# Kernel optimization log

Measured on AMD Instinct MI355X. Metric: run time of the kernel, lower is better.

## Reference

```python
import jax, jax.numpy as jnp
import numpy as np

B, T, M, D, K, L = 128, 50, 4, 64, 64, 16  # batch, seq len, num_beh, embed dim, num_classes, capsule_length
NUM_ITEMS = 100000
R_ITERS = 3


def _dyn_gru(x, C, Wx, bx, Wh, bh):
    """Dynamic capsule GRU. x: [B,M,T,D], C: [B,M,T,K,L] (routing state modulates update gate).
    Returns final hidden beh_e [B,M,K,L] and per-step candidate states beh_N [B,M,T,K,L]."""
    # precompute input projections for all steps: [B,M,T,3,K,L]
    gi = (jnp.einsum('bmtd,mdg->bmtg', x, Wx) + bx[:, None, :]).reshape(x.shape[0], M, T, 3, K, L)

    def step(h, inp):
        gi_t, C_t = inp  # gi_t: [B,M,3,K,L], C_t: [B,M,K,L]
        gh = (jnp.einsum('bmkl,mklg->bmkg', h, Wh) + bh).reshape(h.shape[0], M, K, 3, L)
        r = jax.nn.sigmoid(gi_t[:, :, 0] + gh[:, :, :, 0])
        z = jax.nn.sigmoid(gi_t[:, :, 1] + gh[:, :, :, 1] + C_t)  # dynamic gate via routing state C
        n = jnp.tanh(gi_t[:, :, 2] + r * gh[:, :, :, 2])
        h_new = (1.0 - z) * n + z * h
        return h_new, n

    h0 = jnp.zeros((x.shape[0], M, K, L), x.dtype)
    h_fin, ns = jax.lax.scan(step, h0, (jnp.moveaxis(gi, 2, 0), jnp.moveaxis(C, 2, 0)))
    return h_fin, jnp.moveaxis(ns, 0, 2)


def setup_inputs() -> dict:
    key = jax.random.key(0)
    ks = jax.random.split(key, 9)
    names = ['purchase_seq', 'cart_seq', 'fav_seq', 'click_seq']
    seqs = {n: jax.random.randint(k, (B, T), 0, NUM_ITEMS + 1) for n, k in zip(names, ks[:4])}
    item_emb = jax.random.normal(ks[4], (NUM_ITEMS + 1, D), jnp.float32) * 0.02
    item_emb = item_emb.at[0].set(0.0)  # padding_idx=0
    W = 0.01 * jax.random.uniform(ks[5], (K, L, M, K), jnp.float32)
    W_coef = 0.1 * jax.random.normal(ks[6], (K, D + L, L), jnp.float32)
    alpha = jnp.ones((1,), jnp.float32) * K
    w = jnp.ones((K,), jnp.float32)
    bias = jnp.zeros((K,), jnp.float32)
    gru_Wx = 0.05 * jax.random.normal(ks[7], (M, D, 3 * K * L), jnp.float32)
    gru_bx = jnp.zeros((M, 3 * K * L), jnp.float32)
    gru_Wh = 0.05 * jax.random.normal(ks[8], (M, K, L, 3 * L), jnp.float32)
    gru_bh = jnp.zeros((M, K, 3 * L), jnp.float32)
    return dict(**seqs, item_emb=item_emb, W=W, W_coef=W_coef, alpha=alpha, w=w, bias=bias,
                gru_Wx=gru_Wx, gru_bx=gru_bx, gru_Wh=gru_Wh, gru_bh=gru_bh)


def reference(purchase_seq, cart_seq, fav_seq, click_seq, item_emb, W, W_coef,
              alpha, w, bias, gru_Wx, gru_bx, gru_Wh, gru_bh):
    sg = jax.lax.stop_gradient

    def embed(seq):
        mask = (seq != 0).astype(item_emb.dtype)[..., None]
        return item_emb[seq] * mask

    x = jnp.stack([embed(purchase_seq), embed(cart_seq), embed(fav_seq), embed(click_seq)], axis=1)  # [B,M,T,D]
    bsz = x.shape[0]
    b = jnp.zeros((bsz, K, K, 1), x.dtype)
    C = jnp.zeros((bsz, M, T, K, L), x.dtype)

    # routing iterations (all GRU outputs / W / alpha / w / bias / item_emb detached; W_coef live)
    for _ in range(R_ITERS - 1):
        beh_e, beh_N = _dyn_gru(sg(x), sg(C), sg(gru_Wx), sg(gru_bx), sg(gru_Wh), sg(gru_bh))
        beh_e = sg(beh_e).transpose(0, 2, 1, 3)  # [B,K,M,L]
        u = jnp.einsum('bctd,cdtC->bcCd', beh_e, sg(W))  # [B,K,K,L]
        c = jax.nn.softmax(b, axis=2)
        v = sg(alpha) * jnp.sum(c * u, axis=1)  # [B,K,L]
        v_ = jnp.linalg.norm(v, axis=-1) * sg(w) + sg(bias)  # [B,K]
        E = sg(item_emb)
        p = jax.nn.softmax(v_ @ E.T, axis=-1) @ E  # [B,D]
        p = jnp.broadcast_to(p[:, None, :], (bsz, K, D))
        r = jnp.einsum('bcd,cdD->bcD', jnp.concatenate([p, v], axis=-1), W_coef)  # [B,K,L]
        b = b + jnp.sum(u * r[:, None], axis=-1, keepdims=True)
        C = C + sg(beh_N) * r[:, None, None]

    beh_e, _ = _dyn_gru(x, C, gru_Wx, gru_bx, gru_Wh, gru_bh)
    beh_e = beh_e.transpose(0, 2, 1, 3)
    u_hat = jnp.einsum('bctd,cdtC->bcCd', beh_e, W)
    c = jax.nn.softmax(b, axis=2)
    v = alpha * jnp.sum(c * u_hat, axis=1)
    v_ = jnp.linalg.norm(v, axis=-1) * w + bias
    return v_ @ item_emb.T  # [B, num_items+1]
```

## Files before the change

### kernel.cpp

```cpp
#include <hip/hip_runtime.h>
#include <hip/hip_bf16.h>
#include <cstdint>
#include <cstddef>

#define B_   128
#define T_   50
#define M_   4
#define D_   64
#define K_   64
#define L_   16
#define NIT  100001
#define NBP3 512
#define CHUNK3 196
#define NCH3 7
#define PSTRIDE 8320

typedef unsigned short u16;
typedef unsigned int   u32;
typedef __attribute__((ext_vector_type(8))) short short8;
typedef __attribute__((ext_vector_type(4))) short short4v;
typedef __attribute__((ext_vector_type(4))) float f32x4;

__device__ __forceinline__ float bf2f(u16 v){ u32 u = ((u32)v)<<16; float f; __builtin_memcpy(&f,&u,4); return f; }
__device__ __forceinline__ u16 f2bf(float f){
  u32 u; __builtin_memcpy(&u,&f,4);
  u32 r = (u + 0x7FFFu + ((u>>16)&1u)) >> 16;
  return (u16)r;
}
__device__ __forceinline__ float fexp(float x){ return __builtin_amdgcn_exp2f(x*1.4426950408889634f); }
__device__ __forceinline__ float fsig(float x){ return __builtin_amdgcn_rcpf(1.0f + fexp(-x)); }
__device__ __forceinline__ float ftanh(float x){ return 1.0f - 2.0f*__builtin_amdgcn_rcpf(1.0f + fexp(2.0f*x)); }
__device__ __forceinline__ void unpack8(const u32* s, short8& h, short8& l){
  #pragma unroll
  for (int q=0;q<8;q++){ h[q]=(short)(s[q]&0xFFFFu); l[q]=(short)(s[q]>>16); }
}

#define MFMA32(A,Bv,C) __builtin_amdgcn_mfma_f32_16x16x32_bf16(A,Bv,C,0,0,0)

#if __has_builtin(__builtin_amdgcn_mfma_f32_16x16x16bf16_1k)
__device__ __forceinline__ f32x4 mfma16(short4v a, short4v b, f32x4 c){
  return __builtin_amdgcn_mfma_f32_16x16x16bf16_1k(a,b,c,0,0,0);
}
#elif __has_builtin(__builtin_amdgcn_mfma_f32_16x16x16_bf16)
__device__ __forceinline__ f32x4 mfma16(short4v a, short4v b, f32x4 c){
  return __builtin_amdgcn_mfma_f32_16x16x16_bf16(a,b,c,0,0,0);
}
#else
__device__ __forceinline__ f32x4 mfma16(short4v a, short4v b, f32x4 c){
  asm("v_mfma_f32_16x16x16_bf16 %0, %1, %2, %0" : "+v"(c) : "v"(a), "v"(b));
  return c;
}
#endif

__global__ __launch_bounds__(256) void k_prep_x(const int* __restrict__ s0, const int* __restrict__ s1,
  const int* __restrict__ s2, const int* __restrict__ s3, const float* __restrict__ E,
  u16* __restrict__ xh, u16* __restrict__ xl)
{
  int id = blockIdx.x*256 + threadIdx.x;
  int e8 = id & 7;
  int rm = id >> 3;
  int m = rm / 6400; int r = rm - m*6400;
  int t = r >> 7, b = r & 127;
  const int* sq = (m==0)? s0 : (m==1)? s1 : (m==2)? s2 : s3;
  int idx = sq[b*T_ + t];
  float sc = (idx==0)? 0.0f : 1.0f;
  const float4* ep = (const float4*)(E + (size_t)idx*64 + e8*8);
  float4 v0 = ep[0], v1 = ep[1];
  float vals[8] = {v0.x,v0.y,v0.z,v0.w,v1.x,v1.y,v1.z,v1.w};
  u32 hw[4], lw[4];
  #pragma unroll
  for (int q=0;q<4;q++){
    float f0 = vals[2*q]*sc, f1 = vals[2*q+1]*sc;
    u16 h0 = f2bf(f0), h1 = f2bf(f1);
    u16 l0 = f2bf(f0 - bf2f(h0)), l1 = f2bf(f1 - bf2f(h1));
    hw[q] = (u32)h0 | ((u32)h1<<16);
    lw[q] = (u32)l0 | ((u32)l1<<16);
  }
  size_t off = (size_t)rm*64 + e8*8;
  uint4 hv; hv.x=hw[0]; hv.y=hw[1]; hv.z=hw[2]; hv.w=hw[3];
  uint4 lv; lv.x=lw[0]; lv.y=lw[1]; lv.z=lw[2]; lv.w=lw[3];
  *(uint4*)(xh + off) = hv;
  *(uint4*)(xl + off) = lv;
}

__global__ __launch_bounds__(256) void k_prep_w(const float* __restrict__ Wx,
  u16* __restrict__ wh, u16* __restrict__ wl)
{
  __shared__ float tl[64][65];
  int m = blockIdx.x / 48, gt = blockIdx.x % 48;
  for (int it=0; it<16; ++it){
    int li = threadIdx.x + it*256;
    int dl = li >> 6, gl = li & 63;
    tl[dl][gl] = Wx[((size_t)m*64 + dl)*3072 + gt*64 + gl];
  }
  __syncthreads();
  for (int it=0; it<2; ++it){
    int unit = threadIdx.x + it*256;
    int gl = unit >> 3, d8 = unit & 7;
    u32 hw[4], lw[4];
    #pragma unroll
    for (int q=0;q<4;q++){
      float f0 = tl[d8*8+2*q][gl], f1 = tl[d8*8+2*q+1][gl];
      u16 h0 = f2bf(f0), h1 = f2bf(f1);
      u16 l0 = f2bf(f0 - bf2f(h0)), l1 = f2bf(f1 - bf2f(h1));
      hw[q] = (u32)h0 | ((u32)h1<<16);
      lw[q] = (u32)l0 | ((u32)l1<<16);
    }
    size_t off = ((size_t)m*3072 + gt*64 + gl)*64 + d8*8;
    uint4 hv; hv.x=hw[0]; hv.y=hw[1]; hv.z=hw[2]; hv.w=hw[3];
    uint4 lv; lv.x=lw[0]; lv.y=lw[1]; lv.z=lw[2]; lv.w=lw[3];
    *(uint4*)(wh + off) = hv;
    *(uint4*)(wl + off) = lv;
  }
}

template<int PASS>
__global__ __launch_bounds__(256,2) void k_gru_mfma(
  const u16* __restrict__ xh, const u16* __restrict__ xl,
  const u16* __restrict__ wh, const u16* __restrict__ wl,
  const float* __restrict__ Wh, const float* __restrict__ bx, const float* __restrict__ bhp,
  const float* __restrict__ rp1, const float* __restrict__ rp2,
  const u16* __restrict__ Nr1, const u16* __restrict__ Nr2,
  u16* __restrict__ Nw, float* __restrict__ behE)
{
  int tid = threadIdx.x;
  int lane = tid & 63;
  int n16 = lane & 15, quad = lane >> 4;
  int j0 = quad*4;
  int wid = blockIdx.x*4 + (tid>>6);
  int bt = wid & 7, k = (wid>>3)&63, m = wid>>9;
  int b = bt*16 + n16;

  short8 WxH[3][2], WxL[3][2];
  #pragma unroll
  for (int g=0; g<3; ++g){
    int grow = g*1024 + k*16 + n16;
    #pragma unroll
    for (int c=0; c<2; ++c){
      size_t off = ((size_t)(m*3072 + grow))*64 + c*32 + quad*8;
      WxH[g][c] = *(const short8*)(wh + off);
      WxL[g][c] = *(const short8*)(wl + off);
    }
  }
  const float* whp = Wh + ((size_t)(m*64+k)*16)*48;
  short4v WhH[3], WhL[3];
  #pragma unroll
  for (int g=0; g<3; ++g){
    short4v hhv, llv;
    #pragma unroll
    for (int i=0;i<4;i++){
      float w = whp[(j0+i)*48 + g*16 + n16];
      u16 hbits = f2bf(w);
      hhv[i] = (short)hbits;
      llv[i] = (short)f2bf(w - bf2f(hbits));
    }
    WhH[g]=hhv; WhL[g]=llv;
  }
  float biasv[3][4], bhn[4];
  #pragma unroll
  for (int g=0; g<3; ++g)
    #pragma unroll
    for (int rg=0; rg<4; ++rg){
      int j = j0+rg;
      float tb = bx[m*3072 + g*1024 + k*16 + j];
      if (g<2) tb += bhp[(m*64+k)*48 + g*16 + j];
      biasv[g][rg] = tb;
    }
  #pragma unroll
  for (int rg=0; rg<4; ++rg) bhn[rg] = bhp[(m*64+k)*48 + 32 + j0 + rg];

  float rv1[4]={0.f,0.f,0.f,0.f}, rv2[4]={0.f,0.f,0.f,0.f};
  if (PASS>=2){
    float4 q = *(const float4*)(rp1 + ((size_t)b*64+k)*16 + j0);
    rv1[0]=q.x; rv1[1]=q.y; rv1[2]=q.z; rv1[3]=q.w;
  }
  if (PASS==3){
    float4 q = *(const float4*)(rp2 + ((size_t)b*64+k)*16 + j0);
    rv2[0]=q.x; rv2[1]=q.y; rv2[2]=q.z; rv2[3]=q.w;
  }

  size_t xrow  = ((size_t)m*6400 + bt*16 + n16)*64 + quad*8;
  size_t nbase = ((size_t)(m*64+k))*102400 + (size_t)b*16 + j0;

  short4v hH = {0,0,0,0}, hL = {0,0,0,0};
  float hprev[4] = {0.f,0.f,0.f,0.f};

  short8 A0,A1,A2,A3, Bb0,Bb1,Bb2,Bb3;
  uint2 AN1={0,0}, AN2={0,0}, BN1={0,0}, BN2={0,0};

#define LOADA(tt) { size_t xo = xrow + (size_t)(tt)*8192; \
  A0 = *(const short8*)(xh + xo); A1 = *(const short8*)(xh + xo + 32); \
  A2 = *(const short8*)(xl + xo); A3 = *(const short8*)(xl + xo + 32); \
  if (PASS>=2) AN1 = *(const uint2*)(Nr1 + nbase + (size_t)(tt)*2048); \
  if (PASS==3) AN2 = *(const uint2*)(Nr2 + nbase + (size_t)(tt)*2048); }
#define LOADB(tt) { size_t xo = xrow + (size_t)(tt)*8192; \
  Bb0 = *(const short8*)(xh + xo); Bb1 = *(const short8*)(xh + xo + 32); \
  Bb2 = *(const short8*)(xl + xo); Bb3 = *(const short8*)(xl + xo + 32); \
  if (PASS>=2) BN1 = *(const uint2*)(Nr1 + nbase + (size_t)(tt)*2048); \
  if (PASS==3) BN2 = *(const uint2*)(Nr2 + nbase + (size_t)(tt)*2048); }

#define GRU_STEP(tt, X0,X1,X2,X3, NV1, NV2) { \
  f32x4 giA0 = {biasv[0][0], biasv[0][1], biasv[0][2], biasv[0][3]}; \
  f32x4 giA1 = {biasv[1][0], biasv[1][1], biasv[1][2], biasv[1][3]}; \
  f32x4 giA2 = {biasv[2][0], biasv[2][1], biasv[2][2], biasv[2][3]}; \
  giA0 = MFMA32(WxH[0][0], X0, giA0); giA1 = MFMA32(WxH[1][0], X0, giA1); giA2 = MFMA32(WxH[2][0], X0, giA2); \
  giA0 = MFMA32(WxH[0][1], X1, giA0); giA1 = MFMA32(WxH[1][1], X1, giA1); giA2 = MFMA32(WxH[2][1], X1, giA2); \
  giA0 = MFMA32(WxL[0][0], X0, giA0); giA1 = MFMA32(WxL[1][0], X0, giA1); giA2 = MFMA32(WxL[2][0], X0, giA2); \
  giA0 = MFMA32(WxL[0][1], X1, giA0); giA1 = MFMA32(WxL[1][1], X1, giA1); giA2 = MFMA32(WxL[2][1], X1, giA2); \
  giA0 = MFMA32(WxH[0][0], X2, giA0); giA1 = MFMA32(WxH[1][0], X2, giA1); giA2 = MFMA32(WxH[2][0], X2, giA2); \
  giA0 = MFMA32(WxH[0][1], X3, giA0); giA1 = MFMA32(WxH[1][1], X3, giA1); giA2 = MFMA32(WxH[2][1], X3, giA2); \
  f32x4 ghr = {0.f,0.f,0.f,0.f}, ghz = {0.f,0.f,0.f,0.f}; \
  f32x4 ghn = {bhn[0], bhn[1], bhn[2], bhn[3]}; \
  ghr = mfma16(WhH[0], hH, ghr); ghz = mfma16(WhH[1], hH, ghz); ghn = mfma16(WhH[2], hH, ghn); \
  ghr = mfma16(WhL[0], hH, ghr); ghz = mfma16(WhL[1], hH, ghz); ghn = mfma16(WhL[2], hH, ghn); \
  ghr = mfma16(WhH[0], hL, ghr); ghz = mfma16(WhH[1], hL, ghz); ghn = mfma16(WhH[2], hL, ghn); \
  u32 np0=0, np1=0; \
  short4v hHn = {0,0,0,0}, hLn = {0,0,0,0}; \
  _Pragma("unroll") \
  for (int rg=0; rg<4; ++rg){ \
    float Ct = 0.f; \
    if (PASS>=2){ u32 wb = (rg<2)? NV1.x : NV1.y; Ct = bf2f((u16)(wb >> ((rg&1)*16))) * rv1[rg]; } \
    if (PASS==3){ u32 wb = (rg<2)? NV2.x : NV2.y; Ct += bf2f((u16)(wb >> ((rg&1)*16))) * rv2[rg]; } \
    float rr = fsig(giA0[rg] + ghr[rg]); \
    float zz = fsig(giA1[rg] + ghz[rg] + Ct); \
    float nn = ftanh(giA2[rg] + rr*ghn[rg]); \
    float hvv = nn + zz*(hprev[rg]-nn); \
    hprev[rg] = hvv; \
    if (PASS<=2){ \
      u32 nb = f2bf(nn); \
      if (rg==0) np0 |= nb; else if (rg==1) np0 |= nb<<16; else if (rg==2) np1 |= nb; else np1 |= nb<<16; \
    } \
    u16 hb = f2bf(hvv); \
    hHn[rg] = (short)hb; \
    hLn[rg] = (short)f2bf(hvv - bf2f(hb)); \
  } \
  if (PASS<=2){ uint2 stv; stv.x=np0; stv.y=np1; *(uint2*)(Nw + nbase + (size_t)(tt)*2048) = stv; } \
  hH = hHn; hL = hLn; \
}

  LOADA(0);
  for (int t=0; t<48; t+=2){
    LOADB(t+1);
    GRU_STEP(t,   A0,A1,A2,A3, AN1,AN2);
    LOADA(t+2);
    GRU_STEP(t+1, Bb0,Bb1,Bb2,Bb3, BN1,BN2);
  }
  LOADB(49);
  GRU_STEP(48, A0,A1,A2,A3, AN1,AN2);
  GRU_STEP(49, Bb0,Bb1,Bb2,Bb3, BN1,BN2);
#undef GRU_STEP
#undef LOADA
#undef LOADB

  float4 stv; stv.x=hprev[0]; stv.y=hprev[1]; stv.z=hprev[2]; stv.w=hprev[3];
  *(float4*)(behE + (((size_t)b*64 + k)*4 + m)*16 + j0) = stv;
}

__global__ __launch_bounds__(256) void k_cv(const float* __restrict__ bmat, const float* __restrict__ behE,
  const float* __restrict__ W, const float* __restrict__ alpha, const float* __restrict__ wv,
  const float* __restrict__ bias, float* __restrict__ vout, u32* __restrict__ vBp)
{
  __shared__ float cm[64][65];
  __shared__ float vsh[64][17];
  __shared__ float besh[4096];
  int b = blockIdx.x, tid = threadIdx.x;
  for (int it=0; it<16; ++it){
    int li = tid + it*256;
    cm[li>>6][li&63] = bmat[(size_t)b*4096 + li];
    besh[li] = behE[(size_t)b*4096 + li];
  }
  __syncthreads();
  if (tid < 64){
    float mx = -1e30f;
    for (int jj=0;jj<64;jj++) mx = fmaxf(mx, cm[tid][jj]);
    float sm = 0.f;
    for (int jj=0;jj<64;jj++){ float e = fexp(cm[tid][jj]-mx); cm[tid][jj]=e; sm+=e; }
    float inv = 1.0f/sm;
    for (int jj=0;jj<64;jj++) cm[tid][jj] *= inv;
  }
  __syncthreads();
  int j = tid & 63, dq = tid>>6;
  float a0=0,a1=0,a2=0,a3=0;
  for (int i=0;i<64;++i){
    float cij = cm[i][j];
    #pragma unroll
    for (int q=0;q<4;++q){
      int d = dq*4+q;
      const float* wp = W + ((size_t)((i*16+d)*4))*64 + j;
      float uu = besh[i*64+d]*wp[0] + besh[i*64+16+d]*wp[64]
               + besh[i*64+32+d]*wp[128] + besh[i*64+48+d]*wp[192];
      float cu = cij*uu;
      if (q==0) a0 += cu; else if (q==1) a1 += cu; else if (q==2) a2 += cu; else a3 += cu;
    }
  }
  float al = alpha[0];
  a0*=al; a1*=al; a2*=al; a3*=al;
  vsh[j][dq*4]=a0; vsh[j][dq*4+1]=a1; vsh[j][dq*4+2]=a2; vsh[j][dq*4+3]=a3;
  float* vp = vout + ((size_t)b*64 + j)*16 + dq*4;
  vp[0]=a0; vp[1]=a1; vp[2]=a2; vp[3]=a3;
  __syncthreads();
  if (tid < 64){
    float s=0.f;
    #pragma unroll
    for (int dd=0; dd<16; ++dd){ float q = vsh[tid][dd]; s += q*q; }
    float val = sqrtf(s)*wv[tid] + bias[tid];
    u16 h = f2bf(val); u16 l = f2bf(val - bf2f(h));
    vBp[b*64 + tid] = (u32)h | ((u32)l<<16);
  }
}

__global__ __launch_bounds__(256) void k_pfused(const u32* __restrict__ vBp, const float* __restrict__ E,
  float* __restrict__ partial)
{
  __shared__ u16 etAh[32*72], etAl[32*72];
  __shared__ u16 etBh[64*32], etBl[64*32];
  __shared__ u32 exT[128*36];
  int tid = threadIdx.x, lane = tid&63, w = tid>>6;
  int n16 = lane&15, quad = lane>>4;

  short8 vh[2][2], vl[2][2];
  #pragma unroll
  for (int nt2=0; nt2<2; ++nt2){
    int b = (2*w+nt2)*16 + n16;
    #pragma unroll
    for (int s=0; s<2; ++s){
      u32 tmp[8];
      const u32* src = vBp + b*64 + s*32 + quad*8;
      #pragma unroll
      for (int q=0;q<8;q++) tmp[q]=src[q];
      unpack8(tmp, vh[nt2][s], vl[nt2][s]);
    }
  }
  f32x4 pacc[2][4];
  #pragma unroll
  for (int a2=0;a2<2;a2++)
    #pragma unroll
    for (int b2=0;b2<4;b2++){ pacc[a2][b2][0]=0.f; pacc[a2][b2][1]=0.f; pacc[a2][b2][2]=0.f; pacc[a2][b2][3]=0.f; }
  float srun[2] = {0.f, 0.f};

  int start = blockIdx.x*CHUNK3;
  int bend = start + CHUNK3; if (bend > NIT) bend = NIT;
  int sitem = tid>>3, sc0 = (tid&7)*8;
  for (int ch=0; ch<NCH3; ++ch){
    int i0 = start + ch*32;
    if (i0 >= bend) break;
    {
      int gidx = i0 + sitem;
      float vals[8];
      if (gidx < NIT){
        float4 a = ((const float4*)E)[(size_t)gidx*16 + (sc0>>2)];
        float4 b2 = ((const float4*)E)[(size_t)gidx*16 + (sc0>>2) + 1];
        vals[0]=a.x; vals[1]=a.y; vals[2]=a.z; vals[3]=a.w;
        vals[4]=b2.x; vals[5]=b2.y; vals[6]=b2.z; vals[7]=b2.w;
      } else {
        #pragma unroll
        for (int q=0;q<8;q++) vals[q]=0.f;
      }
      u16 hh[8], ll[8];
      #pragma unroll
      for (int q=0;q<8;q++){ hh[q]=f2bf(vals[q]); ll[q]=f2bf(vals[q]-bf2f(hh[q])); }
      *(short8*)(etAh + sitem*72 + sc0) = *(short8*)hh;
      *(short8*)(etAl + sitem*72 + sc0) = *(short8*)ll;
      #pragma unroll
      for (int q=0;q<8;q++){
        etBh[(sc0+q)*32 + sitem] = hh[q];
        etBl[(sc0+q)*32 + sitem] = ll[q];
      }
    }
    __syncthreads();
    short8 Eh[2][2], El[2][2];
    #pragma unroll
    for (int mt=0; mt<2; ++mt)
      #pragma unroll
      for (int s=0; s<2; ++s){
        Eh[mt][s] = *(const short8*)(etAh + (mt*16 + n16)*72 + s*32 + quad*8);
        El[mt][s] = *(const short8*)(etAl + (mt*16 + n16)*72 + s*32 + quad*8);
      }
    #pragma unroll
    for (int mt=0; mt<2; ++mt){
      #pragma unroll
      for (int nt2=0; nt2<2; ++nt2){
        f32x4 a = {0.f,0.f,0.f,0.f};
        #pragma unroll
        for (int s=0; s<2; ++s){
          a = __builtin_amdgcn_mfma_f32_16x16x32_bf16(Eh[mt][s], vh[nt2][s], a, 0,0,0);
          a = __builtin_amdgcn_mfma_f32_16x16x32_bf16(Eh[mt][s], vl[nt2][s], a, 0,0,0);
          a = __builtin_amdgcn_mfma_f32_16x16x32_bf16(El[mt][s], vh[nt2][s], a, 0,0,0);
        }
        u32 packed[4];
        #pragma unroll
        for (int rg=0; rg<4; ++rg){
          int it_g = i0 + mt*16 + quad*4 + rg;
          float ex = (it_g < bend)? fexp(a[rg]) : 0.f;
          srun[nt2] += ex;
          u16 h = f2bf(ex); u16 l = f2bf(ex - bf2f(h));
          packed[rg] = (u32)h | ((u32)l<<16);
        }
        int bl = (2*w+nt2)*16 + n16;
        uint4 st; st.x=packed[0]; st.y=packed[1]; st.z=packed[2]; st.w=packed[3];
        *(uint4*)(exT + bl*36 + mt*16 + quad*4) = st;
      }
    }
    __syncthreads();
    short8 Xh[2], Xl[2];
    #pragma unroll
    for (int mt2=0; mt2<2; ++mt2){
      int bl = (2*w+mt2)*16 + n16;
      uint4 t0 = *(const uint4*)(exT + bl*36 + quad*8);
      uint4 t1 = *(const uint4*)(exT + bl*36 + quad*8 + 4);
      u32 tmp[8] = {t0.x,t0.y,t0.z,t0.w,t1.x,t1.y,t1.z,t1.w};
      unpack8(tmp, Xh[mt2], Xl[mt2]);
    }
    #pragma unroll
    for (int nt3=0; nt3<4; ++nt3){
      int d = nt3*16 + n16;
      short8 Bh = *(const short8*)(etBh + d*32 + quad*8);
      short8 Bl = *(const short8*)(etBl + d*32 + quad*8);
      #pragma unroll
      for (int mt2=0; mt2<2; ++mt2){
        pacc[mt2][nt3] = __builtin_amdgcn_mfma_f32_16x16x32_bf16(Xh[mt2], Bh, pacc[mt2][nt3], 0,0,0);
        pacc[mt2][nt3] = __builtin_amdgcn_mfma_f32_16x16x32_bf16(Xh[mt2], Bl, pacc[mt2][nt3], 0,0,0);
        pacc[mt2][nt3] = __builtin_amdgcn_mfma_f32_16x16x32_bf16(Xl[mt2], Bh, pacc[mt2][nt3], 0,0,0);
      }
    }
    __syncthreads();
  }
  float* dst = partial + (size_t)blockIdx.x*PSTRIDE;
  #pragma unroll
  for (int mt2=0; mt2<2; ++mt2)
    #pragma unroll
    for (int nt3=0; nt3<4; ++nt3)
      #pragma unroll
      for (int rg=0; rg<4; ++rg){
        int b_g = (2*w+mt2)*16 + quad*4 + rg;
        int d_g = nt3*16 + n16;
        dst[b_g*64 + d_g] = pacc[mt2][nt3][rg];
      }
  #pragma unroll
  for (int nt2=0; nt2<2; ++nt2){
    float vsum = srun[nt2];
    vsum += __shfl_xor(vsum, 16);
    vsum += __shfl_xor(vsum, 32);
    if (quad == 0) dst[8192 + (2*w+nt2)*16 + n16] = vsum;
  }
}

__global__ __launch_bounds__(256) void k_pcomb(const float* __restrict__ partial, float* __restrict__ p)
{
  __shared__ float as_[8][33], ss_[8][33];
  int il = threadIdx.x & 31, qg = threadIdx.x >> 5;
  int id = blockIdx.x*32 + il;
  int b = id >> 6;
  float a = 0.f, s = 0.f;
  for (int q=qg; q<NBP3; q+=8){
    a += partial[(size_t)q*PSTRIDE + id];
    s += partial[(size_t)q*PSTRIDE + 8192 + b];
  }
  as_[qg][il] = a; ss_[qg][il] = s;
  __syncthreads();
  if (qg == 0){
    float at=0.f, st=0.f;
    #pragma unroll
    for (int g=0; g<8; ++g){ at += as_[g][il]; st += ss_[g][il]; }
    p[id] = at/st;
  }
}

__global__ __launch_bounds__(256) void k_r(const float* __restrict__ p, const float* __restrict__ v,
  const float* __restrict__ Wc, float* __restrict__ r, float* __restrict__ rT)
{
  int gid = blockIdx.x*256 + threadIdx.x;
  int l = gid & 15, j = (gid>>4)&63, b = gid>>10;
  const float* wc = Wc + ((size_t)j*80)*16 + l;
  const float* pbp = p + b*64;
  float acc = 0.f;
  #pragma unroll 8
  for (int d=0; d<64; ++d) acc += pbp[d]*wc[d*16];
  const float* vb = v + ((size_t)b*64 + j)*16;
  #pragma unroll
  for (int d=0; d<16; ++d) acc += vb[d]*wc[(64+d)*16];
  r[((size_t)b*64+j)*16 + l] = acc;
  rT[((size_t)b*16+l)*64 + j] = acc;
}

__global__ __launch_bounds__(256) void k_bupd(const float* __restrict__ behE, const float* __restrict__ W,
  const float* __restrict__ rT, float* __restrict__ bmat)
{
  int lane = threadIdx.x & 63;
  int idx = blockIdx.x*4 + (threadIdx.x>>6);
  int b = idx >> 6, i = idx & 63;
  const float* be = behE + (size_t)idx*64;
  const float* rp = rT + (size_t)b*1024;
  float acc = 0.f;
  #pragma unroll
  for (int d=0; d<16; ++d){
    const float* wp = W + ((size_t)((i*16+d)*4))*64 + lane;
    float uu = be[d]*wp[0] + be[16+d]*wp[64] + be[32+d]*wp[128] + be[48+d]*wp[192];
    acc += uu * rp[d*64 + lane];
  }
  bmat[(size_t)idx*64 + lane] += acc;
}

__global__ __launch_bounds__(256) void k_logits(const u32* __restrict__ vBp, const float* __restrict__ E,
  float* __restrict__ out)
{
  __shared__ u16 etAh[64*72], etAl[64*72];
  __shared__ float lt[128*68];
  int tid = threadIdx.x, lane = tid&63, w = tid>>6;
  int n16 = lane&15, quad = lane>>4;
  short8 vh[2][2], vl[2][2];
  #pragma unroll
  for (int nt2=0; nt2<2; ++nt2){
    int b = (2*w+nt2)*16 + n16;
    #pragma unroll
    for (int s=0; s<2; ++s){
      u32 tmp[8];
      const u32* src = vBp + b*64 + s*32 + quad*8;
      #pragma unroll
      for (int q=0;q<8;q++) tmp[q]=src[q];
      unpack8(tmp, vh[nt2][s], vl[nt2][s]);
    }
  }
  int i0 = blockIdx.x*64;
  {
    int sitem = tid>>2, sc0 = (tid&3)*16;
    int gidx = i0 + sitem;
    float vals[16];
    if (gidx < NIT){
      #pragma unroll
      for (int q=0;q<4;q++){
        float4 a = ((const float4*)E)[(size_t)gidx*16 + (sc0>>2) + q];
        vals[4*q]=a.x; vals[4*q+1]=a.y; vals[4*q+2]=a.z; vals[4*q+3]=a.w;
      }
    } else {
      #pragma unroll
      for (int q=0;q<16;q++) vals[q]=0.f;
    }
    u16 hh[16], ll[16];
    #pragma unroll
    for (int q=0;q<16;q++){ hh[q]=f2bf(vals[q]); ll[q]=f2bf(vals[q]-bf2f(hh[q])); }
    *(short8*)(etAh + sitem*72 + sc0)     = *(short8*)hh;
    *(short8*)(etAh + sitem*72 + sc0 + 8) = *(short8*)(hh+8);
    *(short8*)(etAl + sitem*72 + sc0)     = *(short8*)ll;
    *(short8*)(etAl + sitem*72 + sc0 + 8) = *(short8*)(ll+8);
  }
  __syncthreads();
  #pragma unroll
  for (int mt=0; mt<4; ++mt){
    short8 Eh[2], El[2];
    #pragma unroll
    for (int s=0; s<2; ++s){
      Eh[s] = *(const short8*)(etAh + (mt*16 + n16)*72 + s*32 + quad*8);
      El[s] = *(const short8*)(etAl + (mt*16 + n16)*72 + s*32 + quad*8);
    }
    #pragma unroll
    for (int nt2=0; nt2<2; ++nt2){
      f32x4 a = {0.f,0.f,0.f,0.f};
      #pragma unroll
      for (int s=0; s<2; ++s){
        a = __builtin_amdgcn_mfma_f32_16x16x32_bf16(Eh[s], vh[nt2][s], a, 0,0,0);
        a = __builtin_amdgcn_mfma_f32_16x16x32_bf16(Eh[s], vl[nt2][s], a, 0,0,0);
        a = __builtin_amdgcn_mfma_f32_16x16x32_bf16(El[s], vh[nt2][s], a, 0,0,0);
      }
      int b = (2*w+nt2)*16 + n16;
      *(float4*)(lt + b*68 + mt*16 + quad*4) = *(float4*)&a;
    }
  }
  __syncthreads();
  int col = tid & 63, rgp = tid >> 6;
  if (i0 + col < NIT){
    #pragma unroll
    for (int rr=0; rr<32; ++rr){
      int b = rgp*32 + rr;
      out[(size_t)b*NIT + i0 + col] = lt[b*68 + col];
    }
  }
}

extern "C" void kernel_launch(void* const* d_in, const int* in_sizes, int n_in,
                              void* d_out, int out_size, void* d_ws, size_t ws_size,
                              hipStream_t stream)
{
  (void)in_sizes; (void)n_in; (void)out_size; (void)ws_size;
  const int*   s0 = (const int*)d_in[0];
  const int*   s1 = (const int*)d_in[1];
  const int*   s2 = (const int*)d_in[2];
  const int*   s3 = (const int*)d_in[3];
  const float* E  = (const float*)d_in[4];
  const float* W  = (const float*)d_in[5];
  const float* Wc = (const float*)d_in[6];
  const float* alpha = (const float*)d_in[7];
  const float* wv    = (const float*)d_in[8];
  const float* bias  = (const float*)d_in[9];
  const float* Wx = (const float*)d_in[10];
  const float* bx = (const float*)d_in[11];
  const float* Wh = (const float*)d_in[12];
  const float* bh = (const float*)d_in[13];

  char* ws = (char*)d_ws;
  size_t off = 0;
  auto alloc = [&](size_t bytes)->void*{ void* q = ws + off; off += (bytes + 255) & ~(size_t)255; return q; };
  u16*   N1   = (u16*)  alloc((size_t)M_*K_*T_*B_*16*2);
  u16*   N2   = (u16*)  alloc((size_t)M_*K_*T_*B_*16*2);
  u16*   xh   = (u16*)  alloc((size_t)M_*6400*64*2);
  u16*   xl   = (u16*)  alloc((size_t)M_*6400*64*2);
  u16*   wh   = (u16*)  alloc((size_t)M_*3072*64*2);
  u16*   wl   = (u16*)  alloc((size_t)M_*3072*64*2);
  float* bmat = (float*)alloc((size_t)B_*64*64*4);
  float* behE = (float*)alloc((size_t)B_*64*4*16*4);
  float* v    = (float*)alloc((size_t)B_*64*16*4);
  u32*   vBp  = (u32*)  alloc((size_t)128*64*4);
  float* r1   = (float*)alloc((size_t)B_*64*16*4);
  float* rT1  = (float*)alloc((size_t)B_*64*16*4);
  float* r2   = (float*)alloc((size_t)B_*64*16*4);
  float* rT2  = (float*)alloc((size_t)B_*64*16*4);
  float* p    = (float*)alloc((size_t)B_*64*4);
  float* partial = (float*)alloc((size_t)NBP3*PSTRIDE*4);

  hipMemsetAsync(bmat, 0, (size_t)B_*64*64*4, stream);
  k_prep_x<<<800,256,0,stream>>>(s0,s1,s2,s3,E,xh,xl);
  k_prep_w<<<192,256,0,stream>>>(Wx,wh,wl);

  k_gru_mfma<1><<<512,256,0,stream>>>(xh,xl,wh,wl,Wh,bx,bh,
                                      nullptr,nullptr,nullptr,nullptr, N1, behE);
  k_cv<<<128,256,0,stream>>>(bmat,behE,W,alpha,wv,bias,v,vBp);
  k_pfused<<<NBP3,256,0,stream>>>(vBp,E,partial);
  k_pcomb<<<256,256,0,stream>>>(partial,p);
  k_r<<<512,256,0,stream>>>(p,v,Wc,r1,rT1);
  k_bupd<<<2048,256,0,stream>>>(behE,W,rT1,bmat);

  k_gru_mfma<2><<<512,256,0,stream>>>(xh,xl,wh,wl,Wh,bx,bh,
                                      r1,nullptr, N1,nullptr, N2, behE);
  k_cv<<<128,256,0,stream>>>(bmat,behE,W,alpha,wv,bias,v,vBp);
  k_pfused<<<NBP3,256,0,stream>>>(vBp,E,partial);
  k_pcomb<<<256,256,0,stream>>>(partial,p);
  k_r<<<512,256,0,stream>>>(p,v,Wc,r2,rT2);
  k_bupd<<<2048,256,0,stream>>>(behE,W,rT2,bmat);

  k_gru_mfma<3><<<512,256,0,stream>>>(xh,xl,wh,wl,Wh,bx,bh,
                                      r1,r2, N1,N2, nullptr, behE);
  k_cv<<<128,256,0,stream>>>(bmat,behE,W,alpha,wv,bias,v,vBp);
  k_logits<<<1563,256,0,stream>>>(vBp,E,(float*)d_out);
}
```

Measured before the change: 483.1 us.

## Fuse partial reduction with r projection, prefetch E chunks, parallelize softmax

Merges the partial-sum combine kernel and the W_coef projection kernel into one per-batch kernel, which removes a launch and the round trip of p through global memory on each of the two routing iterations. In the p-softmax kernel the next 32-item chunk of E is loaded into registers before the current chunk is processed, so global load latency overlaps the MFMA work. The row softmax in k_cv now uses all 256 threads, splitting each row into four slices with shared-memory max and sum reductions, instead of 64 threads doing serial loops. The fused kernel runs only 128 blocks, which lowers parallelism for the r computation.

```diff
diff --git a/kernel.cpp b/kernel.cpp
--- a/kernel.cpp
+++ b/kernel.cpp
@@ -263,6 +263,7 @@
   __shared__ float cm[64][65];
   __shared__ float vsh[64][17];
   __shared__ float besh[4096];
+  __shared__ float smx[4][64], ssm[4][64];
   int b = blockIdx.x, tid = threadIdx.x;
   for (int it=0; it<16; ++it){
     int li = tid + it*256;
@@ -270,13 +271,23 @@
     besh[li] = behE[(size_t)b*4096 + li];
   }
   __syncthreads();
-  if (tid < 64){
+  {
+    int row = tid & 63, sl = tid >> 6;
+    int c0 = sl*16;
     float mx = -1e30f;
-    for (int jj=0;jj<64;jj++) mx = fmaxf(mx, cm[tid][jj]);
+    #pragma unroll
+    for (int c=0;c<16;c++) mx = fmaxf(mx, cm[row][c0+c]);
+    smx[sl][row] = mx;
+    __syncthreads();
+    float m4 = fmaxf(fmaxf(smx[0][row],smx[1][row]), fmaxf(smx[2][row],smx[3][row]));
     float sm = 0.f;
-    for (int jj=0;jj<64;jj++){ float e = fexp(cm[tid][jj]-mx); cm[tid][jj]=e; sm+=e; }
-    float inv = 1.0f/sm;
-    for (int jj=0;jj<64;jj++) cm[tid][jj] *= inv;
+    #pragma unroll
+    for (int c=0;c<16;c++){ float e = fexp(cm[row][c0+c]-m4); cm[row][c0+c]=e; sm+=e; }
+    ssm[sl][row] = sm;
+    __syncthreads();
+    float inv = 1.0f/(ssm[0][row]+ssm[1][row]+ssm[2][row]+ssm[3][row]);
+    #pragma unroll
+    for (int c=0;c<16;c++) cm[row][c0+c] *= inv;
   }
   __syncthreads();
   int j = tid & 63, dq = tid>>6;
@@ -341,24 +352,24 @@
   int start = blockIdx.x*CHUNK3;
   int bend = start + CHUNK3; if (bend > NIT) bend = NIT;
   int sitem = tid>>3, sc0 = (tid&7)*8;
+
+  float vals[8]; float mk;
+  {
+    int gidx = start + sitem;
+    int ga = (gidx < NIT) ? gidx : 0;
+    mk = (gidx < NIT) ? 1.f : 0.f;
+    float4 a = ((const float4*)E)[(size_t)ga*16 + (sc0>>2)];
+    float4 b2 = ((const float4*)E)[(size_t)ga*16 + (sc0>>2) + 1];
+    vals[0]=a.x; vals[1]=a.y; vals[2]=a.z; vals[3]=a.w;
+    vals[4]=b2.x; vals[5]=b2.y; vals[6]=b2.z; vals[7]=b2.w;
+  }
   for (int ch=0; ch<NCH3; ++ch){
     int i0 = start + ch*32;
     if (i0 >= bend) break;
     {
-      int gidx = i0 + sitem;
-      float vals[8];
-      if (gidx < NIT){
-        float4 a = ((const float4*)E)[(size_t)gidx*16 + (sc0>>2)];
-        float4 b2 = ((const float4*)E)[(size_t)gidx*16 + (sc0>>2) + 1];
-        vals[0]=a.x; vals[1]=a.y; vals[2]=a.z; vals[3]=a.w;
-        vals[4]=b2.x; vals[5]=b2.y; vals[6]=b2.z; vals[7]=b2.w;
-      } else {
-        #pragma unroll
-        for (int q=0;q<8;q++) vals[q]=0.f;
-      }
       u16 hh[8], ll[8];
       #pragma unroll
-      for (int q=0;q<8;q++){ hh[q]=f2bf(vals[q]); ll[q]=f2bf(vals[q]-bf2f(hh[q])); }
+      for (int q=0;q<8;q++){ float vq = vals[q]*mk; hh[q]=f2bf(vq); ll[q]=f2bf(vq-bf2f(hh[q])); }
       *(short8*)(etAh + sitem*72 + sc0) = *(short8*)hh;
       *(short8*)(etAl + sitem*72 + sc0) = *(short8*)ll;
       #pragma unroll
@@ -368,6 +379,15 @@
       }
     }
     __syncthreads();
+    {
+      int gidx = i0 + 32 + sitem;
+      int ga = (gidx < NIT) ? gidx : 0;
+      mk = (gidx < NIT) ? 1.f : 0.f;
+      float4 a = ((const float4*)E)[(size_t)ga*16 + (sc0>>2)];
+      float4 b2 = ((const float4*)E)[(size_t)ga*16 + (sc0>>2) + 1];
+      vals[0]=a.x; vals[1]=a.y; vals[2]=a.z; vals[3]=a.w;
+      vals[4]=b2.x; vals[5]=b2.y; vals[6]=b2.z; vals[7]=b2.w;
+    }
     short8 Eh[2][2], El[2][2];
     #pragma unroll
     for (int mt=0; mt<2; ++mt)
@@ -445,42 +465,44 @@
   }
 }
 
-__global__ __launch_bounds__(256) void k_pcomb(const float* __restrict__ partial, float* __restrict__ p)
-{
-  __shared__ float as_[8][33], ss_[8][33];
-  int il = threadIdx.x & 31, qg = threadIdx.x >> 5;
-  int id = blockIdx.x*32 + il;
-  int b = id >> 6;
-  float a = 0.f, s = 0.f;
-  for (int q=qg; q<NBP3; q+=8){
-    a += partial[(size_t)q*PSTRIDE + id];
-    s += partial[(size_t)q*PSTRIDE + 8192 + b];
-  }
-  as_[qg][il] = a; ss_[qg][il] = s;
-  __syncthreads();
-  if (qg == 0){
-    float at=0.f, st=0.f;
-    #pragma unroll
-    for (int g=0; g<8; ++g){ at += as_[g][il]; st += ss_[g][il]; }
-    p[id] = at/st;
-  }
-}
-
-__global__ __launch_bounds__(256) void k_r(const float* __restrict__ p, const float* __restrict__ v,
-  const float* __restrict__ Wc, float* __restrict__ r, float* __restrict__ rT)
-{
-  int gid = blockIdx.x*256 + threadIdx.x;
-  int l = gid & 15, j = (gid>>4)&63, b = gid>>10;
-  const float* wc = Wc + ((size_t)j*80)*16 + l;
-  const float* pbp = p + b*64;
-  float acc = 0.f;
-  #pragma unroll 8
-  for (int d=0; d<64; ++d) acc += pbp[d]*wc[d*16];
-  const float* vb = v + ((size_t)b*64 + j)*16;
-  #pragma unroll
-  for (int d=0; d<16; ++d) acc += vb[d]*wc[(64+d)*16];
-  r[((size_t)b*64+j)*16 + l] = acc;
-  rT[((size_t)b*16+l)*64 + j] = acc;
+__global__ __launch_bounds__(256) void k_pcr(const float* __restrict__ partial,
+  const float* __restrict__ v, const float* __restrict__ Wc,
+  float* __restrict__ r, float* __restrict__ rT)
+{
+  __shared__ float ared[4][64];
+  __shared__ float sred[256];
+  __shared__ float psh[64];
+  int b = blockIdx.x, tid = threadIdx.x;
+  int d = tid & 63, qs = tid >> 6;
+  float a = 0.f;
+  for (int q = qs; q < NBP3; q += 4)
+    a += partial[(size_t)q*PSTRIDE + b*64 + d];
+  ared[qs][d] = a;
+  sred[tid] = partial[(size_t)tid*PSTRIDE + 8192 + b]
+            + partial[(size_t)(tid+256)*PSTRIDE + 8192 + b];
+  __syncthreads();
+  if (tid < 64){
+    float sv = sred[tid] + sred[tid+64] + sred[tid+128] + sred[tid+192];
+    sv += __shfl_xor(sv, 1);  sv += __shfl_xor(sv, 2);  sv += __shfl_xor(sv, 4);
+    sv += __shfl_xor(sv, 8);  sv += __shfl_xor(sv, 16); sv += __shfl_xor(sv, 32);
+    float at = ared[0][tid]+ared[1][tid]+ared[2][tid]+ared[3][tid];
+    psh[tid] = at / sv;
+  }
+  __syncthreads();
+  int l = tid & 15, jbase = tid >> 4;
+  #pragma unroll
+  for (int jb=0; jb<4; ++jb){
+    int j = jb*16 + jbase;
+    const float* wc = Wc + ((size_t)j*80)*16 + l;
+    float acc = 0.f;
+    #pragma unroll 8
+    for (int dd=0; dd<64; ++dd) acc += psh[dd]*wc[dd*16];
+    const float* vb = v + ((size_t)b*64 + j)*16;
+    #pragma unroll
+    for (int dd=0; dd<16; ++dd) acc += vb[dd]*wc[(64+dd)*16];
+    r[((size_t)b*64+j)*16 + l] = acc;
+    rT[((size_t)b*16+l)*64 + j] = acc;
+  }
 }
 
 __global__ __launch_bounds__(256) void k_bupd(const float* __restrict__ behE, const float* __restrict__ W,
@@ -614,7 +636,6 @@
   float* rT1  = (float*)alloc((size_t)B_*64*16*4);
   float* r2   = (float*)alloc((size_t)B_*64*16*4);
   float* rT2  = (float*)alloc((size_t)B_*64*16*4);
-  float* p    = (float*)alloc((size_t)B_*64*4);
   float* partial = (float*)alloc((size_t)NBP3*PSTRIDE*4);
 
   hipMemsetAsync(bmat, 0, (size_t)B_*64*64*4, stream);
@@ -625,16 +646,14 @@
                                       nullptr,nullptr,nullptr,nullptr, N1, behE);
   k_cv<<<128,256,0,stream>>>(bmat,behE,W,alpha,wv,bias,v,vBp);
   k_pfused<<<NBP3,256,0,stream>>>(vBp,E,partial);
-  k_pcomb<<<256,256,0,stream>>>(partial,p);
-  k_r<<<512,256,0,stream>>>(p,v,Wc,r1,rT1);
+  k_pcr<<<128,256,0,stream>>>(partial,v,Wc,r1,rT1);
   k_bupd<<<2048,256,0,stream>>>(behE,W,rT1,bmat);
 
   k_gru_mfma<2><<<512,256,0,stream>>>(xh,xl,wh,wl,Wh,bx,bh,
                                       r1,nullptr, N1,nullptr, N2, behE);
   k_cv<<<128,256,0,stream>>>(bmat,behE,W,alpha,wv,bias,v,vBp);
   k_pfused<<<NBP3,256,0,stream>>>(vBp,E,partial);
-  k_pcomb<<<256,256,0,stream>>>(partial,p);
-  k_r<<<512,256,0,stream>>>(p,v,Wc,r2,rT2);
+  k_pcr<<<128,256,0,stream>>>(partial,v,Wc,r2,rT2);
   k_bupd<<<2048,256,0,stream>>>(behE,W,rT2,bmat);
 
   k_gru_mfma<3><<<512,256,0,stream>>>(xh,xl,wh,wl,Wh,bx,bh,
```

New measurement: 513.2 us. 6.2% more time.
